# Kernel optimization log

Measured on AMD Instinct MI355X. Metric: run time of the kernel, lower is better.

Reference implementation:

```python
import jax, jax.numpy as jnp
import numpy as np

N, D = 8192, 512  # scaled from hardcoded 1140, 100


def setup_inputs() -> dict:
    key = jax.random.key(0)
    ks = jax.random.split(key, 7)
    return {
        "U": jax.random.uniform(ks[0], (N, N), jnp.float32),
        "X": jax.random.uniform(ks[1], (N, N), jnp.float32),
        # learned params (torch init was uniform[0,1) for H_1/W0/W1; Linear uses kaiming-ish)
        "H_1": jax.random.uniform(ks[2], (N, D), jnp.float32),
        "W0": jax.random.uniform(ks[3], (N, D), jnp.float32),
        "W1": jax.random.uniform(ks[4], (D, N), jnp.float32),
        "Wa": jax.random.normal(ks[5], (D, N), jnp.float32) * (1.0 / np.sqrt(N)),
        "ba": jnp.zeros((D,), jnp.float32),
    }


def reference(U, X, H_1, W0, W1, Wa, ba):
    # Per-row attention loop, fully vectorized.
    # Note: in the original, att_layer(A2[i]) reads row i BEFORE it is overwritten,
    # so K is computed from the unmodified U (A2 = U / 1).
    K = jnp.tanh(U @ Wa.T + ba)                 # [N, D]  (Linear + Tanh)
    S = jax.nn.softmax(K @ H_1.T, axis=1)       # [N, N]  row i: softmax(H_1 @ K_i)
    S = jax.lax.stop_gradient(S)                # torch: score.detach().numpy() round-trip
    A2 = U * S                                  # [N, N]  elementwise re-weighted rows
    # encoder: nn.Softmax() on 2D input defaults to dim=1
    Z = jax.nn.softmax(A2 @ X @ W0, axis=1)     # [N, D]
    # decoder: Sigmoid
    X_p = jax.nn.sigmoid(U @ Z @ W1)            # [N, N]
    return (X_p, Z)
```

## Files before the change

kernel.cpp:

```cpp
#include <hip/hip_runtime.h>
#include <math.h>


typedef __attribute__((ext_vector_type(8))) short bf16x8;
typedef __attribute__((ext_vector_type(8))) _Float16 f16x8;
typedef __attribute__((ext_vector_type(4))) float f32x4;
typedef __attribute__((ext_vector_type(4))) unsigned short us4;

__device__ __forceinline__ unsigned short f2h(float x) {
    _Float16 h = (_Float16)x;
    return __builtin_bit_cast(unsigned short, h);
}
__device__ __forceinline__ float h2f(unsigned short u) {
    return (float)__builtin_bit_cast(_Float16, u);
}

__device__ __forceinline__ void gload_lds16(const char* g, char* l) {
    __builtin_amdgcn_global_load_lds(
        (const __attribute__((address_space(1))) unsigned int*)g,
        (__attribute__((address_space(3))) unsigned int*)l, 16, 0, 0);
}

__device__ __forceinline__ int swz(int o) {
    return o ^ (((o >> 7) & 7) << 4);
}

__device__ __forceinline__ f32x4 mfma16(bf16x8 a, bf16x8 b, f32x4 c) {
    return __builtin_amdgcn_mfma_f32_16x16x32_f16(
        __builtin_bit_cast(f16x8, a), __builtin_bit_cast(f16x8, b), c, 0, 0, 0);
}

__global__ __launch_bounds__(256)
void convert_f16(const float* __restrict__ in, unsigned short* __restrict__ hi, size_t n)
{
    size_t i = ((size_t)blockIdx.x * blockDim.x + threadIdx.x) * 4;
    const size_t stride = (size_t)gridDim.x * blockDim.x * 4;
    for (; i < n; i += stride) {
        float4 v = *(const float4*)(in + i);
        us4 h;
        h.x = f2h(v.x); h.y = f2h(v.y); h.z = f2h(v.z); h.w = f2h(v.w);
        *(us4*)(hi + i) = h;
    }
}

template<bool CSUB>
__global__ __launch_bounds__(256)
void transpose_cvt(const float* __restrict__ in, unsigned short* __restrict__ hi,
                   const float* __restrict__ cvec, int R, int C)
{
    __shared__ float tile[32][33];
    const int t = threadIdx.x, tx = t & 31, ty = t >> 5;
    const int c0 = blockIdx.x * 32, r0 = blockIdx.y * 32;
#pragma unroll
    for (int i = 0; i < 4; ++i)
        tile[ty + 8 * i][tx] = in[(size_t)(r0 + ty + 8 * i) * C + c0 + tx];
    __syncthreads();
#pragma unroll
    for (int i = 0; i < 4; ++i) {
        const int col = c0 + ty + 8 * i;
        float v = tile[tx][ty + 8 * i];
        if (CSUB) v -= cvec[col];
        hi[(size_t)col * R + r0 + tx] = f2h(v);
    }
}

__global__ __launch_bounds__(256)
void colsum512(const float* __restrict__ in, float* __restrict__ c, int Nrows)
{
    const int t = threadIdx.x;
    const int r0 = blockIdx.x * 16;
    float s0 = 0.f, s1 = 0.f;
    for (int r = 0; r < 16; ++r) {
        const float* row = in + (size_t)(r0 + r) * 512;
        s0 += row[t];
        s1 += row[t + 256];
    }
    atomicAdd(&c[t], s0);
    atomicAdd(&c[t + 256], s1);
}

__global__ void scale_vec(float* __restrict__ c, float s, int n)
{
    const int t = threadIdx.x;
    if (t < n) c[t] *= s;
}

template<int FM, int WM, int WN, int EPI>
__global__ __launch_bounds__(WM * WN * 64)
void gemm_mfma(const unsigned short* __restrict__ Ahi,
               const unsigned short* __restrict__ Bh, float* __restrict__ Cf,
               unsigned short* __restrict__ Ch,
               int M, int Ncol, int Kdim)
{
    constexpr int NWAVES = WM * WN;
    constexpr int BM = WM * FM * 16;
    constexpr int BN = WN * 64;
    constexpr int ABYTES = BM * 64;
    constexpr int BBYTES = BN * 64;
    constexpr int LDSB = ABYTES + BBYTES;
    constexpr int CPW = LDSB / 1024 / NWAVES;

    __shared__ __align__(1024) char lds[2][LDSB];

    const int t = threadIdx.x;
    const int w = t >> 6, lane = t & 63;

    const int gx = gridDim.x;
    const int nwg = gx * gridDim.y;
    const int lid = blockIdx.y * gx + blockIdx.x;
    const int tl = (lid & 7) * (nwg >> 3) + (lid >> 3);
    const int m0 = (tl / gx) * BM, n0 = (tl % gx) * BN;

    const int kseg = Kdim / gridDim.z;
    const int kbeg = blockIdx.z * kseg;
    const int ksteps = kseg >> 5;
    const size_t zoff = (size_t)blockIdx.z * ((size_t)M * Ncol);

    const int wr = w / WN, wc = w % WN;
    const int l15 = lane & 15, kq = lane >> 4;

    const char* gsrc[CPW];
    int lofs[CPW];
#pragma unroll
    for (int c = 0; c < CPW; ++c) {
        const int boff = (w * CPW + c) * 1024;
        lofs[c] = boff;
        const int poff = swz(boff + lane * 16);
        const unsigned short* mat;
        int moff, rbase;
        if (poff < ABYTES) { mat = Ahi; moff = poff;          rbase = m0; }
        else               { mat = Bh;  moff = poff - ABYTES; rbase = n0; }
        gsrc[c] = (const char*)(mat + (size_t)(rbase + (moff >> 6)) * Kdim + kbeg) + (moff & 63);
    }

    int aoffS[FM], boffS[4];
#pragma unroll
    for (int m = 0; m < FM; ++m)
        aoffS[m] = swz((wr * (FM * 16) + m * 16 + l15) * 64 + kq * 16);
#pragma unroll
    for (int n = 0; n < 4; ++n)
        boffS[n] = swz(ABYTES + (wc * 64 + n * 16 + l15) * 64 + kq * 16);

    f32x4 acc[FM][4];
#pragma unroll
    for (int m = 0; m < FM; ++m)
#pragma unroll
        for (int n = 0; n < 4; ++n)
            acc[m][n] = (f32x4)(0.f);

    auto stage = [&](int buf) {
#pragma unroll
        for (int c = 0; c < CPW; ++c) {
            gload_lds16(gsrc[c], &lds[buf][lofs[c]]);
            gsrc[c] += 64;
        }
    };

    stage(0);
    __syncthreads();

    int cur = 0;
    for (int ks = 0; ks < ksteps; ++ks) {
        if (ks + 1 < ksteps) stage(cur ^ 1);

        const char* Lb = lds[cur];
        bf16x8 ah[FM], bb[4];
#pragma unroll
        for (int m = 0; m < FM; ++m)
            ah[m] = *(const bf16x8*)(Lb + aoffS[m]);
#pragma unroll
        for (int n = 0; n < 4; ++n)
            bb[n] = *(const bf16x8*)(Lb + boffS[n]);

        __builtin_amdgcn_s_setprio(1);
#pragma unroll
        for (int n = 0; n < 4; ++n)
#pragma unroll
            for (int m = 0; m < FM; ++m)
                acc[m][n] = mfma16(ah[m], bb[n], acc[m][n]);
        __builtin_amdgcn_s_setprio(0);

        __syncthreads();
        cur ^= 1;
    }

#pragma unroll
    for (int m = 0; m < FM; ++m) {
        const int rowb = m0 + wr * (FM * 16) + m * 16 + kq * 4;
#pragma unroll
        for (int n = 0; n < 4; ++n) {
            const int col = n0 + wc * 64 + n * 16 + l15;
#pragma unroll
            for (int r = 0; r < 4; ++r) {
                float v = acc[m][n][r];
                const size_t idx = (size_t)(rowb + r) * Ncol + col;
                if constexpr (EPI == 0) {
                    Cf[zoff + idx] = v;
                } else if constexpr (EPI == 2) {
                    Cf[idx] = 1.f / (1.f + __expf(-v));
                } else {
                    Ch[idx] = f2h(v);
                }
            }
        }
    }
}

template<int RED>
__global__ __launch_bounds__(256)
void reduce_splitk(const float* __restrict__ P, size_t seg,
                   const float* __restrict__ ba, const float* __restrict__ rs,
                   const float* __restrict__ cv, float scale, int Ncol,
                   float* __restrict__ outf, unsigned short* __restrict__ outh)
{
    const size_t i = ((size_t)blockIdx.x * blockDim.x + threadIdx.x) * 4;
    float4 a = *(const float4*)(P + i);
    float4 b = *(const float4*)(P + seg + i);
    float4 c = *(const float4*)(P + 2 * seg + i);
    float4 d = *(const float4*)(P + 3 * seg + i);
    float s0 = a.x + b.x + c.x + d.x;
    float s1 = a.y + b.y + c.y + d.y;
    float s2 = a.z + b.z + c.z + d.z;
    float s3 = a.w + b.w + c.w + d.w;
    const int col = (int)(i % (size_t)Ncol);

    if constexpr (RED == 0) {
        us4 h;
        h.x = f2h(tanhf(s0 + ba[col + 0]));
        h.y = f2h(tanhf(s1 + ba[col + 1]));
        h.z = f2h(tanhf(s2 + ba[col + 2]));
        h.w = f2h(tanhf(s3 + ba[col + 3]));
        *(us4*)(outh + i) = h;
    } else if constexpr (RED == 1) {
        float4 o; o.x = s0; o.y = s1; o.z = s2; o.w = s3;
        *(float4*)(outf + i) = o;
    } else if constexpr (RED == 2) {
        const float rsr = rs[i / (size_t)Ncol];
        float4 o;
        o.x = s0 * scale + rsr * cv[col + 0];
        o.y = s1 * scale + rsr * cv[col + 1];
        o.z = s2 * scale + rsr * cv[col + 2];
        o.w = s3 * scale + rsr * cv[col + 3];
        *(float4*)(outf + i) = o;
    } else {
        us4 h;
        h.x = f2h(s0); h.y = f2h(s1); h.z = f2h(s2); h.w = f2h(s3);
        *(us4*)(outh + i) = h;
    }
}

__device__ inline float blockReduceMax(float v, float* sred)
{
    for (int o = 32; o > 0; o >>= 1) v = fmaxf(v, __shfl_down(v, o));
    const int lane = threadIdx.x & 63, wid = threadIdx.x >> 6;
    if (lane == 0) sred[wid] = v;
    __syncthreads();
    if (threadIdx.x == 0) {
        float m = sred[0];
        for (int w = 1; w < 4; ++w) m = fmaxf(m, sred[w]);
        sred[0] = m;
    }
    __syncthreads();
    float r = sred[0];
    __syncthreads();
    return r;
}

__device__ inline float blockReduceSum(float v, float* sred)
{
    for (int o = 32; o > 0; o >>= 1) v += __shfl_down(v, o);
    const int lane = threadIdx.x & 63, wid = threadIdx.x >> 6;
    if (lane == 0) sred[wid] = v;
    __syncthreads();
    if (threadIdx.x == 0) {
        float m = sred[0];
        for (int w = 1; w < 4; ++w) m += sred[w];
        sred[0] = m;
    }
    __syncthreads();
    float r = sred[0];
    __syncthreads();
    return r;
}

__global__ __launch_bounds__(256)
void softmax_mul_f16s(const unsigned short* __restrict__ Lrow,
                      const unsigned short* __restrict__ Uh,
                      unsigned short* __restrict__ hi, float* __restrict__ rowsum, int Ncols)
{
    __shared__ float srow[8192];
    __shared__ float sred[8];
    const int t = threadIdx.x;
    const size_t base = (size_t)blockIdx.x * Ncols;

    float lmax = -3.402823466e38f;
    for (int c = t * 4; c < Ncols; c += 1024) {
        us4 lv = *(const us4*)(Lrow + base + c);
        float4 v;
        v.x = h2f(lv.x); v.y = h2f(lv.y); v.z = h2f(lv.z); v.w = h2f(lv.w);
        *(float4*)&srow[c] = v;
        lmax = fmaxf(lmax, fmaxf(fmaxf(v.x, v.y), fmaxf(v.z, v.w)));
    }
    const float rmax = blockReduceMax(lmax, sred);

    float lsum = 0.f;
    for (int c = t * 4; c < Ncols; c += 1024) {
        float4 v = *(float4*)&srow[c];
        v.x = __expf(v.x - rmax);
        v.y = __expf(v.y - rmax);
        v.z = __expf(v.z - rmax);
        v.w = __expf(v.w - rmax);
        *(float4*)&srow[c] = v;
        lsum += v.x + v.y + v.z + v.w;
    }
    const float rsum = blockReduceSum(lsum, sred);
    const float inv = 1.f / rsum;

    float a2sum = 0.f;
    for (int c = t * 4; c < Ncols; c += 1024) {
        float4 e = *(float4*)&srow[c];
        us4 u = *(const us4*)(Uh + base + c);
        float a0 = h2f(u.x) * e.x * inv, a1 = h2f(u.y) * e.y * inv;
        float a2 = h2f(u.z) * e.z * inv, a3 = h2f(u.w) * e.w * inv;
        a2sum += a0 + a1 + a2 + a3;
        us4 h;
        h.x = f2h(a0 * 1024.f);
        h.y = f2h(a1 * 1024.f);
        h.z = f2h(a2 * 1024.f);
        h.w = f2h(a3 * 1024.f);
        *(us4*)(hi + base + c) = h;
    }
    const float rssum = blockReduceSum(a2sum, sred);
    if (t == 0) rowsum[blockIdx.x] = rssum;
}

__global__ __launch_bounds__(256)
void softmax16_t(float* __restrict__ buf, unsigned short* __restrict__ zt, int N)
{
    __shared__ float s[16][513];
    const int t = threadIdx.x, lane = t & 63, wid = t >> 6;
    const int r0 = blockIdx.x * 16;

#pragma unroll
    for (int i = 0; i < 8; ++i) {
        const int flat = i * 256 + t;
        const int row = flat >> 7;
        const int c4 = (flat & 127) * 4;
        float4 v = *(const float4*)(buf + (size_t)(r0 + row) * 512 + c4);
        s[row][c4 + 0] = v.x; s[row][c4 + 1] = v.y;
        s[row][c4 + 2] = v.z; s[row][c4 + 3] = v.w;
    }
    __syncthreads();

#pragma unroll
    for (int rr = 0; rr < 4; ++rr) {
        const int row = wid * 4 + rr;
        float vals[8];
        float m = -3.402823466e38f;
#pragma unroll
        for (int j = 0; j < 8; ++j) { vals[j] = s[row][lane * 8 + j]; m = fmaxf(m, vals[j]); }
#pragma unroll
        for (int o = 32; o > 0; o >>= 1) m = fmaxf(m, __shfl_xor(m, o));
        float sum = 0.f;
#pragma unroll
        for (int j = 0; j < 8; ++j) { vals[j] = __expf(vals[j] - m); sum += vals[j]; }
#pragma unroll
        for (int o = 32; o > 0; o >>= 1) sum += __shfl_xor(sum, o);
        const float inv = 1.f / sum;
        float4 o1, o2;
        o1.x = vals[0] * inv; o1.y = vals[1] * inv; o1.z = vals[2] * inv; o1.w = vals[3] * inv;
        o2.x = vals[4] * inv; o2.y = vals[5] * inv; o2.z = vals[6] * inv; o2.w = vals[7] * inv;
        s[row][lane * 8 + 0] = o1.x; s[row][lane * 8 + 1] = o1.y;
        s[row][lane * 8 + 2] = o1.z; s[row][lane * 8 + 3] = o1.w;
        s[row][lane * 8 + 4] = o2.x; s[row][lane * 8 + 5] = o2.y;
        s[row][lane * 8 + 6] = o2.z; s[row][lane * 8 + 7] = o2.w;
        *(float4*)(buf + (size_t)(r0 + row) * 512 + lane * 8) = o1;
        *(float4*)(buf + (size_t)(r0 + row) * 512 + lane * 8 + 4) = o2;
    }
    __syncthreads();

#pragma unroll
    for (int cc = 0; cc < 2; ++cc) {
        const int col = t * 2 + cc;
        unsigned short tmp[16];
#pragma unroll
        for (int row = 0; row < 16; ++row) tmp[row] = f2h(s[row][col]);
#pragma unroll
        for (int q = 0; q < 4; ++q)
            *(us4*)(zt + (size_t)col * N + r0 + q * 4) = *(us4*)&tmp[q * 4];
    }
}

__global__ __launch_bounds__(256)
void softmax_inplace_small(float* buf, int D)
{
    __shared__ float sred[8];
    const int t = threadIdx.x;
    const size_t base = (size_t)blockIdx.x * D;
    float2 v = *(float2*)(buf + base + t * 2);
    const float rmax = blockReduceMax(fmaxf(v.x, v.y), sred);
    const float e0 = __expf(v.x - rmax);
    const float e1 = __expf(v.y - rmax);
    const float rsum = blockReduceSum(e0 + e1, sred);
    const float inv = 1.f / rsum;
    float2 o;
    o.x = e0 * inv;
    o.y = e1 * inv;
    *(float2*)(buf + base + t * 2) = o;
}

template<int EPI, bool TB>
__global__ __launch_bounds__(256)
void gemm_f32(const float* __restrict__ A, const float* __restrict__ B,
              const float* __restrict__ bias, float* __restrict__ C,
              int M, int Ncol, int Kdim)
{
    constexpr int FBM = 128, FBN = 128, FBK = 8;
    __shared__ float As[FBK][FBM];
    __shared__ float Bs[FBK][FBN];
    const int t  = threadIdx.x;
    const int tx = t & 15, ty = t >> 4;
    const int m0 = blockIdx.y * FBM, n0 = blockIdx.x * FBN;

    const int arow  = t >> 1;
    const int acol4 = (t & 1) * 4;
    const int brow  = t >> 5;
    const int bcol4 = (t & 31) * 4;

    float acc[8][8];
#pragma unroll
    for (int i = 0; i < 8; ++i)
#pragma unroll
        for (int j = 0; j < 8; ++j) acc[i][j] = 0.f;

    const float* Aptr = A + (size_t)(m0 + arow) * Kdim + acol4;
    const float* Bptr;
    if (TB) Bptr = B + (size_t)(n0 + arow) * Kdim + acol4;
    else    Bptr = B + (size_t)brow * Ncol + n0 + bcol4;

    float4 av = *(const float4*)(Aptr);
    float4 bv = *(const float4*)(Bptr);

    for (int k0 = 0; k0 < Kdim; k0 += FBK) {
        As[acol4 + 0][arow] = av.x;
        As[acol4 + 1][arow] = av.y;
        As[acol4 + 2][arow] = av.z;
        As[acol4 + 3][arow] = av.w;
        if (TB) {
            Bs[acol4 + 0][arow] = bv.x;
            Bs[acol4 + 1][arow] = bv.y;
            Bs[acol4 + 2][arow] = bv.z;
            Bs[acol4 + 3][arow] = bv.w;
        } else {
            *(float4*)&Bs[brow][bcol4] = bv;
        }
        __syncthreads();

        if (k0 + FBK < Kdim) {
            av = *(const float4*)(Aptr + (k0 + FBK));
            if (TB) bv = *(const float4*)(Bptr + (k0 + FBK));
            else    bv = *(const float4*)(Bptr + (size_t)(k0 + FBK) * Ncol);
        }

#pragma unroll
        for (int kk = 0; kk < FBK; ++kk) {
            float a[8], b[8];
            *(float4*)&a[0] = *(const float4*)&As[kk][ty * 4];
            *(float4*)&a[4] = *(const float4*)&As[kk][64 + ty * 4];
            *(float4*)&b[0] = *(const float4*)&Bs[kk][tx * 4];
            *(float4*)&b[4] = *(const float4*)&Bs[kk][64 + tx * 4];
#pragma unroll
            for (int i = 0; i < 8; ++i)
#pragma unroll
                for (int j = 0; j < 8; ++j)
                    acc[i][j] = fmaf(a[i], b[j], acc[i][j]);
        }
        __syncthreads();
    }

#pragma unroll
    for (int ib = 0; ib < 2; ++ib) {
#pragma unroll
        for (int ii = 0; ii < 4; ++ii) {
            const int i = ib * 4 + ii;
            const size_t row = (size_t)(m0 + ib * 64 + ty * 4 + ii);
            float* crow = C + row * (size_t)Ncol;
#pragma unroll
            for (int jb = 0; jb < 2; ++jb) {
                const int col0 = n0 + jb * 64 + tx * 4;
                float4 v;
                v.x = acc[i][jb * 4 + 0];
                v.y = acc[i][jb * 4 + 1];
                v.z = acc[i][jb * 4 + 2];
                v.w = acc[i][jb * 4 + 3];
                if (EPI == 1) {
                    v.x = tanhf(v.x + bias[col0 + 0]);
                    v.y = tanhf(v.y + bias[col0 + 1]);
                    v.z = tanhf(v.z + bias[col0 + 2]);
                    v.w = tanhf(v.w + bias[col0 + 3]);
                } else if (EPI == 2) {
                    v.x = 1.f / (1.f + __expf(-v.x));
                    v.y = 1.f / (1.f + __expf(-v.y));
                    v.z = 1.f / (1.f + __expf(-v.z));
                    v.w = 1.f / (1.f + __expf(-v.w));
                }
                *(float4*)(crow + col0) = v;
            }
        }
    }
}

__global__ __launch_bounds__(256)
void softmax_mul_f32(float* buf, const float* __restrict__ U, int Ncols)
{
    __shared__ float srow[8192];
    __shared__ float sred[8];
    const int t = threadIdx.x;
    const size_t base = (size_t)blockIdx.x * Ncols;

    float lmax = -3.402823466e38f;
    for (int c = t * 4; c < Ncols; c += 1024) {
        float4 v = *(const float4*)(buf + base + c);
        *(float4*)&srow[c] = v;
        lmax = fmaxf(lmax, fmaxf(fmaxf(v.x, v.y), fmaxf(v.z, v.w)));
    }
    const float rmax = blockReduceMax(lmax, sred);

    float lsum = 0.f;
    for (int c = t * 4; c < Ncols; c += 1024) {
        float4 v = *(float4*)&srow[c];
        v.x = __expf(v.x - rmax);
        v.y = __expf(v.y - rmax);
        v.z = __expf(v.z - rmax);
        v.w = __expf(v.w - rmax);
        *(float4*)&srow[c] = v;
        lsum += v.x + v.y + v.z + v.w;
    }
    const float rsum = blockReduceSum(lsum, sred);
    const float inv = 1.f / rsum;

    for (int c = t * 4; c < Ncols; c += 1024) {
        float4 e = *(float4*)&srow[c];
        float4 u = *(const float4*)(U + base + c);
        float4 o;
        o.x = u.x * e.x * inv;
        o.y = u.y * e.y * inv;
        o.z = u.z * e.z * inv;
        o.w = u.w * e.w * inv;
        *(float4*)(buf + base + c) = o;
    }
}

extern "C" void kernel_launch(void* const* d_in, const int* in_sizes, int n_in,
                              void* d_out, int out_size, void* d_ws, size_t ws_size,
                              hipStream_t stream)
{
    const float* U  = (const float*)d_in[0];
    const float* X  = (const float*)d_in[1];
    const float* H1 = (const float*)d_in[2];
    const float* W0 = (const float*)d_in[3];
    const float* W1 = (const float*)d_in[4];
    const float* Wa = (const float*)d_in[5];
    const float* ba = (const float*)d_in[6];
    const int D = in_sizes[6];
    const int N = (int)((long long)in_sizes[2] / D);
    const size_t NN = (size_t)N * N, ND = (size_t)N * D;

    float* Xp = (float*)d_out;
    float* Zp = Xp + NN;

    char* p = (char*)d_ws;
    auto alloc = [&](size_t bytes) { char* r = p; p += (bytes + 255) & ~(size_t)255; return r; };
    unsigned short* wa_h  = (unsigned short*)alloc(ND * 2);
    unsigned short* h1_h  = (unsigned short*)alloc(ND * 2);
    unsigned short* k_h   = (unsigned short*)alloc(ND * 2);
    unsigned short* w0t_h = (unsigned short*)alloc(ND * 2);
    unsigned short* vbt   = (unsigned short*)alloc(ND * 2);
    unsigned short* zt_h  = (unsigned short*)alloc(ND * 2);
    unsigned short* uz_h  = (unsigned short*)alloc(ND * 2);
    unsigned short* w1t_h = (unsigned short*)alloc(ND * 2);
    float*          xw0f  = (float*)alloc(ND * 4);
    float*          cvec  = (float*)alloc((size_t)D * 4);
    float*          rsum  = (float*)alloc((size_t)N * 4);
    float*          Pp    = (float*)alloc(ND * 4 * 4);
    unsigned short* Uh    = (unsigned short*)alloc(NN * 2);
    unsigned short* Xh    = (unsigned short*)alloc(NN * 2);
    const size_t need = (size_t)(p - (char*)d_ws);

    dim3 blk(256), blk512(512);

    if (N == 8192 && D == 512 && ws_size >= need) {
        unsigned short* Lh = (unsigned short*)Xp;
        const dim3 gSlimK(D / 128, N / 128, 4);
        const dim3 gBig(N / 256, N / 128);
        const dim3 gT(D / 32, N / 32);
        const dim3 gTw1(N / 32, D / 32);
        const dim3 gRed((unsigned)(ND / 1024));
        const int cgrid = 4096;
        unsigned short* nullw = nullptr;
        const float* nullf = nullptr;

        hipLaunchKernelGGL(convert_f16, dim3(cgrid), blk, 0, stream, U, Uh, NN);
        hipLaunchKernelGGL(convert_f16, dim3(1024), blk, 0, stream, Wa, wa_h, ND);
        hipLaunchKernelGGL((gemm_mfma<4, 2, 2, 0>), gSlimK, blk, 0, stream,
                           Uh, wa_h, Pp, nullw, N, D, N);
        hipLaunchKernelGGL((reduce_splitk<0>), gRed, blk, 0, stream,
                           Pp, ND, ba, nullf, nullf, 0.f, D, (float*)nullptr, k_h);
        hipLaunchKernelGGL(convert_f16, dim3(1024), blk, 0, stream, H1, h1_h, ND);
        hipLaunchKernelGGL((gemm_mfma<4, 2, 4, 3>), gBig, blk512, 0, stream,
                           k_h, h1_h, (float*)nullptr, Lh, N, N, D);
        hipLaunchKernelGGL(convert_f16, dim3(cgrid), blk, 0, stream, X, Xh, NN);
        hipLaunchKernelGGL((transpose_cvt<false>), gT, blk, 0, stream, W0, w0t_h, nullf, N, D);
        hipLaunchKernelGGL((gemm_mfma<4, 2, 2, 0>), gSlimK, blk, 0, stream,
                           Xh, w0t_h, Pp, nullw, N, D, N);
        hipLaunchKernelGGL((reduce_splitk<1>), gRed, blk, 0, stream,
                           Pp, ND, nullf, nullf, nullf, 0.f, D, xw0f, nullw);
        hipMemsetAsync(cvec, 0, (size_t)D * 4, stream);
        hipLaunchKernelGGL(colsum512, dim3(N / 16), blk, 0, stream, xw0f, cvec, N);
        hipLaunchKernelGGL(scale_vec, dim3(1), dim3(512), 0, stream, cvec, 1.0f / (float)N, D);
        hipLaunchKernelGGL((transpose_cvt<true>), gT, blk, 0, stream, xw0f, vbt, cvec, N, D);
        hipLaunchKernelGGL(softmax_mul_f16s, dim3(N), blk, 0, stream, Lh, Uh, Xh, rsum, N);
        hipLaunchKernelGGL((gemm_mfma<4, 2, 2, 0>), gSlimK, blk, 0, stream,
                           Xh, vbt, Pp, nullw, N, D, N);
        hipLaunchKernelGGL((reduce_splitk<2>), gRed, blk, 0, stream,
                           Pp, ND, nullf, rsum, cvec, 1.0f / 1024.f, D, Zp, nullw);
        hipLaunchKernelGGL(softmax16_t, dim3(N / 16), blk, 0, stream, Zp, zt_h, N);
        hipLaunchKernelGGL((gemm_mfma<4, 2, 2, 0>), gSlimK, blk, 0, stream,
                           Uh, zt_h, Pp, nullw, N, D, N);
        hipLaunchKernelGGL((reduce_splitk<3>), gRed, blk, 0, stream,
                           Pp, ND, nullf, nullf, nullf, 0.f, D, (float*)nullptr, uz_h);
        hipLaunchKernelGGL((transpose_cvt<false>), gTw1, blk, 0, stream, W1, w1t_h, nullf, D, N);
        hipLaunchKernelGGL((gemm_mfma<4, 2, 4, 2>), gBig, blk512, 0, stream,
                           uz_h, w1t_h, Xp, nullw, N, N, D);
    } else {
        float* bufA = (float*)d_ws;
        dim3 gD(D / 128, N / 128);
        dim3 gN(N / 128, N / 128);
        hipLaunchKernelGGL((gemm_f32<1, true>),  gD, blk, 0, stream, U,    Wa, ba,      bufA, N, D, N);
        hipLaunchKernelGGL((gemm_f32<0, true>),  gN, blk, 0, stream, bufA, H1, nullptr, Xp,   N, N, D);
        hipLaunchKernelGGL(softmax_mul_f32, dim3(N), blk, 0, stream, Xp, U, N);
        hipLaunchKernelGGL((gemm_f32<0, false>), gD, blk, 0, stream, X,    W0, nullptr, bufA, N, D, N);
        hipLaunchKernelGGL((gemm_f32<0, false>), gD, blk, 0, stream, Xp,   bufA, nullptr, Zp, N, D, N);
        hipLaunchKernelGGL(softmax_inplace_small, dim3(N), blk, 0, stream, Zp, D);
        hipLaunchKernelGGL((gemm_f32<0, false>), gD, blk, 0, stream, U,    Zp, nullptr, bufA, N, D, N);
        hipLaunchKernelGGL((gemm_f32<2, false>), gN, blk, 0, stream, bufA, W1, nullptr, Xp,  N, N, D);
    }
}
```

Before: 1.029 ms.

## Add 256x256 eight-wave ping-pong MFMA GEMM with 128KB LDS pipelining

Introduces a new gemm8p kernel using 512 threads, 256x256 output tiles, double-buffered 128KB LDS with direct global-to-LDS loads, staged prefetch interleaved with MFMA phases, s_setprio and explicit vmcnt waits. It replaces the split-K slim GEMMs and both big N x N GEMMs, with a fallback to the old kernel if the dynamic LDS attribute cannot be set. The intent is higher MFMA utilization by overlapping loads with compute and increasing per-tile reuse. The risk is that the slim GEMMs now launch fewer workgroups (2x32x4 = 256) at one block per CU, and the hand-tuned vmcnt counts are fragile.

```diff
diff --git a/kernel.cpp b/kernel.cpp
--- a/kernel.cpp
+++ b/kernel.cpp
@@ -24,10 +24,175 @@
 __device__ __forceinline__ int swz(int o) {
     return o ^ (((o >> 7) & 7) << 4);
 }
+__device__ __forceinline__ int swzk(int o) {
+    return o ^ (((o >> 7) & 3) << 4);
+}
 
 __device__ __forceinline__ f32x4 mfma16(bf16x8 a, bf16x8 b, f32x4 c) {
     return __builtin_amdgcn_mfma_f32_16x16x32_f16(
         __builtin_bit_cast(f16x8, a), __builtin_bit_cast(f16x8, b), c, 0, 0, 0);
+}
+
+template<int EPI>
+__global__ __launch_bounds__(512, 1)
+void gemm8p(const unsigned short* __restrict__ A, const unsigned short* __restrict__ B,
+            float* __restrict__ Cf, unsigned short* __restrict__ Ch,
+            int M, int Ncol, int Kdim)
+{
+    extern __shared__ char lds[];
+    constexpr int RSZ = 16384;
+
+    const int tid = threadIdx.x;
+    const int w = tid >> 6, lane = tid & 63;
+    const int wr = w >> 2, wc = w & 3;
+    const int l15 = lane & 15, kq = lane >> 4;
+
+    const int gx = gridDim.x;
+    const int nwg = gx * gridDim.y;
+    const int lid = blockIdx.y * gx + blockIdx.x;
+    const int tl = (lid & 7) * (nwg >> 3) + (lid >> 3);
+    const int m0 = (tl / gx) * 256, n0 = (tl % gx) * 256;
+
+    const int kseg = Kdim / gridDim.z;
+    const int kbeg = blockIdx.z * kseg;
+    const int T = kseg >> 6;
+    const size_t zoff = (size_t)blockIdx.z * ((size_t)M * Ncol);
+
+    const int Kb = Kdim * 2;
+    const char* gp[4][2];
+    {
+        const char* Ab = (const char*)A + (size_t)m0 * Kb + (size_t)kbeg * 2;
+        const char* Bb = (const char*)B + (size_t)n0 * Kb + (size_t)kbeg * 2;
+#pragma unroll
+        for (int r = 0; r < 4; ++r) {
+            const char* base = (r < 2) ? Ab : Bb;
+            const int khalf = r & 1;
+#pragma unroll
+            for (int j = 0; j < 2; ++j) {
+                const int moff = swzk((w * 2 + j) * 1024 + lane * 16);
+                gp[r][j] = base + (size_t)(moff >> 6) * Kb + khalf * 64 + (moff & 63);
+            }
+        }
+    }
+
+    auto stage = [&](int r, int tile) {
+        char* dst = lds + (tile & 1) * 65536 + r * RSZ + w * 2048;
+        gload_lds16(gp[r][0] + (size_t)tile * 128, dst);
+        gload_lds16(gp[r][1] + (size_t)tile * 128, dst + 1024);
+    };
+
+    int aoff[8], boff[4];
+#pragma unroll
+    for (int mf = 0; mf < 8; ++mf)
+        aoff[mf] = swzk((wr * 128 + mf * 16 + l15) * 64 + kq * 16);
+#pragma unroll
+    for (int n = 0; n < 4; ++n)
+        boff[n] = swzk((wc * 64 + n * 16 + l15) * 64 + kq * 16);
+
+    f32x4 acc[8][4];
+#pragma unroll
+    for (int m = 0; m < 8; ++m)
+#pragma unroll
+        for (int n = 0; n < 4; ++n)
+            acc[m][n] = (f32x4)(0.f);
+
+    stage(2, 0); stage(0, 0); stage(3, 0); stage(1, 0);
+    stage(2, 1); stage(0, 1); stage(3, 1);
+    asm volatile("s_waitcnt vmcnt(10)" ::: "memory");
+    __builtin_amdgcn_s_barrier();
+
+    for (int t = 0; t < T; ++t) {
+        const char* Lb = lds + (t & 1) * 65536;
+        bf16x8 bfr[4], afr[4];
+
+#pragma unroll
+        for (int n = 0; n < 4; ++n) bfr[n] = *(const bf16x8*)(Lb + 2 * RSZ + boff[n]);
+#pragma unroll
+        for (int m = 0; m < 4; ++m) afr[m] = *(const bf16x8*)(Lb + 0 * RSZ + aoff[m]);
+        if (t + 1 < T) stage(1, t + 1);
+        __builtin_amdgcn_s_barrier();
+        __builtin_amdgcn_s_setprio(1);
+#pragma unroll
+        for (int n = 0; n < 4; ++n)
+#pragma unroll
+            for (int m = 0; m < 4; ++m)
+                acc[m][n] = mfma16(afr[m], bfr[n], acc[m][n]);
+        __builtin_amdgcn_s_setprio(0);
+        __builtin_amdgcn_sched_barrier(0);
+        __builtin_amdgcn_s_barrier();
+
+#pragma unroll
+        for (int m = 0; m < 4; ++m) afr[m] = *(const bf16x8*)(Lb + 0 * RSZ + aoff[4 + m]);
+        if (t + 2 < T) stage(2, t + 2);
+        __builtin_amdgcn_s_barrier();
+        __builtin_amdgcn_s_setprio(1);
+#pragma unroll
+        for (int n = 0; n < 4; ++n)
+#pragma unroll
+            for (int m = 0; m < 4; ++m)
+                acc[4 + m][n] = mfma16(afr[m], bfr[n], acc[4 + m][n]);
+        __builtin_amdgcn_s_setprio(0);
+        __builtin_amdgcn_sched_barrier(0);
+        if (t < T - 2)       { asm volatile("s_waitcnt vmcnt(10)" ::: "memory"); }
+        else if (t == T - 2) { asm volatile("s_waitcnt vmcnt(8)"  ::: "memory"); }
+        else                 { asm volatile("s_waitcnt vmcnt(0)"  ::: "memory"); }
+        __builtin_amdgcn_s_barrier();
+
+#pragma unroll
+        for (int n = 0; n < 4; ++n) bfr[n] = *(const bf16x8*)(Lb + 3 * RSZ + boff[n]);
+#pragma unroll
+        for (int m = 0; m < 4; ++m) afr[m] = *(const bf16x8*)(Lb + 1 * RSZ + aoff[m]);
+        if (t + 2 < T) stage(0, t + 2);
+        __builtin_amdgcn_s_barrier();
+        __builtin_amdgcn_s_setprio(1);
+#pragma unroll
+        for (int n = 0; n < 4; ++n)
+#pragma unroll
+            for (int m = 0; m < 4; ++m)
+                acc[m][n] = mfma16(afr[m], bfr[n], acc[m][n]);
+        __builtin_amdgcn_s_setprio(0);
+        __builtin_amdgcn_sched_barrier(0);
+        __builtin_amdgcn_s_barrier();
+
+#pragma unroll
+        for (int m = 0; m < 4; ++m) afr[m] = *(const bf16x8*)(Lb + 1 * RSZ + aoff[4 + m]);
+        if (t + 2 < T) stage(3, t + 2);
+        __builtin_amdgcn_s_barrier();
+        __builtin_amdgcn_s_setprio(1);
+#pragma unroll
+        for (int n = 0; n < 4; ++n)
+#pragma unroll
+            for (int m = 0; m < 4; ++m)
+                acc[4 + m][n] = mfma16(afr[m], bfr[n], acc[4 + m][n]);
+        __builtin_amdgcn_s_setprio(0);
+        __builtin_amdgcn_sched_barrier(0);
+        if (t + 1 < T) {
+            if (t + 2 < T) { asm volatile("s_waitcnt vmcnt(10)" ::: "memory"); }
+            else           { asm volatile("s_waitcnt vmcnt(4)"  ::: "memory"); }
+        }
+        __builtin_amdgcn_s_barrier();
+    }
+
+#pragma unroll
+    for (int m = 0; m < 8; ++m) {
+        const int rowb = m0 + wr * 128 + m * 16 + kq * 4;
+#pragma unroll
+        for (int n = 0; n < 4; ++n) {
+            const int col = n0 + wc * 64 + n * 16 + l15;
+#pragma unroll
+            for (int r = 0; r < 4; ++r) {
+                float v = acc[m][n][r];
+                const size_t idx = (size_t)(rowb + r) * Ncol + col;
+                if constexpr (EPI == 0) {
+                    Cf[zoff + idx] = v;
+                } else if constexpr (EPI == 2) {
+                    Cf[idx] = 1.f / (1.f + __expf(-v));
+                } else {
+                    Ch[idx] = f2h(v);
+                }
+            }
+        }
+    }
 }
 
 __global__ __launch_bounds__(256)
@@ -590,7 +755,18 @@
     dim3 blk(256), blk512(512);
 
     if (N == 8192 && D == 512 && ws_size >= need) {
+        constexpr int LDS8P = 131072;
+        bool ok8p = true;
+        ok8p &= hipFuncSetAttribute((const void*)gemm8p<0>,
+                    hipFuncAttributeMaxDynamicSharedMemorySize, LDS8P) == hipSuccess;
+        ok8p &= hipFuncSetAttribute((const void*)gemm8p<2>,
+                    hipFuncAttributeMaxDynamicSharedMemorySize, LDS8P) == hipSuccess;
+        ok8p &= hipFuncSetAttribute((const void*)gemm8p<3>,
+                    hipFuncAttributeMaxDynamicSharedMemorySize, LDS8P) == hipSuccess;
+
         unsigned short* Lh = (unsigned short*)Xp;
+        const dim3 gSlim8(D / 256, N / 256, 4);
+        const dim3 gBig8(N / 256, N / 256);
         const dim3 gSlimK(D / 128, N / 128, 4);
         const dim3 gBig(N / 256, N / 128);
         const dim3 gT(D / 32, N / 32);
@@ -600,19 +776,30 @@
         unsigned short* nullw = nullptr;
         const float* nullf = nullptr;
 
+        auto slimGemm = [&](const unsigned short* A_, const unsigned short* B_, float* C_) {
+            if (ok8p)
+                hipLaunchKernelGGL((gemm8p<0>), gSlim8, blk512, LDS8P, stream,
+                                   A_, B_, C_, nullw, N, D, N);
+            else
+                hipLaunchKernelGGL((gemm_mfma<4, 2, 2, 0>), gSlimK, blk, 0, stream,
+                                   A_, B_, C_, nullw, N, D, N);
+        };
+
         hipLaunchKernelGGL(convert_f16, dim3(cgrid), blk, 0, stream, U, Uh, NN);
         hipLaunchKernelGGL(convert_f16, dim3(1024), blk, 0, stream, Wa, wa_h, ND);
-        hipLaunchKernelGGL((gemm_mfma<4, 2, 2, 0>), gSlimK, blk, 0, stream,
-                           Uh, wa_h, Pp, nullw, N, D, N);
+        slimGemm(Uh, wa_h, Pp);
         hipLaunchKernelGGL((reduce_splitk<0>), gRed, blk, 0, stream,
                            Pp, ND, ba, nullf, nullf, 0.f, D, (float*)nullptr, k_h);
         hipLaunchKernelGGL(convert_f16, dim3(1024), blk, 0, stream, H1, h1_h, ND);
-        hipLaunchKernelGGL((gemm_mfma<4, 2, 4, 3>), gBig, blk512, 0, stream,
-                           k_h, h1_h, (float*)nullptr, Lh, N, N, D);
+        if (ok8p)
+            hipLaunchKernelGGL((gemm8p<3>), gBig8, blk512, LDS8P, stream,
+                               k_h, h1_h, (float*)nullptr, Lh, N, N, D);
+        else
+            hipLaunchKernelGGL((gemm_mfma<4, 2, 4, 3>), gBig, blk512, 0, stream,
+                               k_h, h1_h, (float*)nullptr, Lh, N, N, D);
         hipLaunchKernelGGL(convert_f16, dim3(cgrid), blk, 0, stream, X, Xh, NN);
         hipLaunchKernelGGL((transpose_cvt<false>), gT, blk, 0, stream, W0, w0t_h, nullf, N, D);
-        hipLaunchKernelGGL((gemm_mfma<4, 2, 2, 0>), gSlimK, blk, 0, stream,
-                           Xh, w0t_h, Pp, nullw, N, D, N);
+        slimGemm(Xh, w0t_h, Pp);
         hipLaunchKernelGGL((reduce_splitk<1>), gRed, blk, 0, stream,
                            Pp, ND, nullf, nullf, nullf, 0.f, D, xw0f, nullw);
         hipMemsetAsync(cvec, 0, (size_t)D * 4, stream);
@@ -620,18 +807,20 @@
         hipLaunchKernelGGL(scale_vec, dim3(1), dim3(512), 0, stream, cvec, 1.0f / (float)N, D);
         hipLaunchKernelGGL((transpose_cvt<true>), gT, blk, 0, stream, xw0f, vbt, cvec, N, D);
         hipLaunchKernelGGL(softmax_mul_f16s, dim3(N), blk, 0, stream, Lh, Uh, Xh, rsum, N);
-        hipLaunchKernelGGL((gemm_mfma<4, 2, 2, 0>), gSlimK, blk, 0, stream,
-                           Xh, vbt, Pp, nullw, N, D, N);
+        slimGemm(Xh, vbt, Pp);
         hipLaunchKernelGGL((reduce_splitk<2>), gRed, blk, 0, stream,
                            Pp, ND, nullf, rsum, cvec, 1.0f / 1024.f, D, Zp, nullw);
         hipLaunchKernelGGL(softmax16_t, dim3(N / 16), blk, 0, stream, Zp, zt_h, N);
-        hipLaunchKernelGGL((gemm_mfma<4, 2, 2, 0>), gSlimK, blk, 0, stream,
-                           Uh, zt_h, Pp, nullw, N, D, N);
+        slimGemm(Uh, zt_h, Pp);
         hipLaunchKernelGGL((reduce_splitk<3>), gRed, blk, 0, stream,
                            Pp, ND, nullf, nullf, nullf, 0.f, D, (float*)nullptr, uz_h);
         hipLaunchKernelGGL((transpose_cvt<false>), gTw1, blk, 0, stream, W1, w1t_h, nullf, D, N);
-        hipLaunchKernelGGL((gemm_mfma<4, 2, 4, 2>), gBig, blk512, 0, stream,
-                           uz_h, w1t_h, Xp, nullw, N, N, D);
+        if (ok8p)
+            hipLaunchKernelGGL((gemm8p<2>), gBig8, blk512, LDS8P, stream,
+                               uz_h, w1t_h, Xp, nullw, N, N, D);
+        else
+            hipLaunchKernelGGL((gemm_mfma<4, 2, 4, 2>), gBig, blk512, 0, stream,
+                               uz_h, w1t_h, Xp, nullw, N, N, D);
     } else {
         float* bufA = (float*)d_ws;
         dim3 gD(D / 128, N / 128);
```

After: 913.1 us. -11.2%, faster.
